# Kernel optimization log

Measured on AMD Instinct MI355X. Metric: run time of the kernel, lower is better.

The kernel has to match this reference:

```python
import jax, jax.numpy as jnp
import numpy as np

NUM_POINTS = 10


def _notaknot_spline_coeffs(points, values):
    """Replicates scipy.interpolate.CubicSpline (bc_type='not-a-knot').
    Solves for knot slopes s, then per-interval cubic coeffs in t = x - x_i:
      y = c3*t^3 + c2*t^2 + c1*t + c0.
    n = 10 so the dense n x n solve is negligible."""
    n = points.shape[0]
    dx = jnp.diff(points)                     # [n-1]
    slope = jnp.diff(values) / dx             # [n-1]

    A = jnp.zeros((n, n), dtype=points.dtype)
    b = jnp.zeros((n,), dtype=points.dtype)
    idx = jnp.arange(1, n - 1)
    # interior continuity-of-second-derivative rows
    A = A.at[idx, idx - 1].set(dx[1:])
    A = A.at[idx, idx].set(2.0 * (dx[:-1] + dx[1:]))
    A = A.at[idx, idx + 1].set(dx[:-1])
    b = b.at[idx].set(3.0 * (dx[1:] * slope[:-1] + dx[:-1] * slope[1:]))
    # not-a-knot boundary rows (as in scipy CubicSpline source)
    d0 = points[2] - points[0]
    A = A.at[0, 0].set(dx[1])
    A = A.at[0, 1].set(d0)
    b = b.at[0].set(((dx[0] + 2.0 * d0) * dx[1] * slope[0] + dx[0] ** 2 * slope[1]) / d0)
    dn = points[-1] - points[-3]
    A = A.at[-1, -1].set(dx[-2])
    A = A.at[-1, -2].set(dn)
    b = b.at[-1].set((dx[-1] ** 2 * slope[-2] + (2.0 * dn + dx[-1]) * dx[-2] * slope[-1]) / dn)

    s = jnp.linalg.solve(A, b)                # knot first derivatives
    t = (s[:-1] + s[1:] - 2.0 * slope) / dx
    c3 = t / dx
    c2 = (slope - s[:-1]) / dx - t
    c1 = s[:-1]
    c0 = values[:-1]
    return c3, c2, c1, c0


def setup_inputs() -> dict:
    key = jax.random.key(0)
    kx, kv = jax.random.split(key)
    x = jax.random.uniform(kx, (4096, 4096), dtype=jnp.float32)  # in [0,1) subset of [-1,1]
    points = jnp.linspace(-1.0, 1.0, NUM_POINTS, dtype=jnp.float32)  # nn.Parameter init
    values = jax.random.normal(kv, (NUM_POINTS,), dtype=jnp.float32)
    return {"x": x, "points": points, "values": values}


def reference(x, points, values):
    c3, c2, c1, c0 = _notaknot_spline_coeffs(points, values)
    xf = x.ravel()
    # interval search; clip -> end-interval polynomials extrapolate (scipy default)
    i = jnp.clip(jnp.searchsorted(points, xf, side='right') - 1, 0, points.shape[0] - 2)
    t = xf - points[i]
    y = ((c3[i] * t + c2[i]) * t + c1[i]) * t + c0[i]  # Horner
    return y.reshape(x.shape)
```

## Files before the change

kernel.cpp:

```cpp
#include <hip/hip_runtime.h>

typedef float float4v __attribute__((ext_vector_type(4)));

#define BLOCK 256

__device__ __forceinline__ void spline_setup(const float* __restrict__ points,
                                             const float* __restrict__ values,
                                             float2* s32, float2* s10, float* sm)
{
    float p[10], v[10];
#pragma unroll
    for (int k = 0; k < 10; ++k) { p[k] = points[k]; v[k] = values[k]; }
    float dx[9], sl[9];
#pragma unroll
    for (int k = 0; k < 9; ++k) { dx[k] = p[k + 1] - p[k]; sl[k] = (v[k + 1] - v[k]) / dx[k]; }

    float dg[10], lo[10], up[10], bb[10];
    float d0 = p[2] - p[0];
    dg[0] = dx[1]; up[0] = d0; lo[0] = 0.0f;
    bb[0] = ((dx[0] + 2.0f * d0) * dx[1] * sl[0] + dx[0] * dx[0] * sl[1]) / d0;
#pragma unroll
    for (int i = 1; i <= 8; ++i) {
        lo[i] = dx[i];
        dg[i] = 2.0f * (dx[i - 1] + dx[i]);
        up[i] = dx[i - 1];
        bb[i] = 3.0f * (dx[i] * sl[i - 1] + dx[i - 1] * sl[i]);
    }
    float dn = p[9] - p[7];
    lo[9] = dn; dg[9] = dx[7]; up[9] = 0.0f;
    bb[9] = (dx[8] * dx[8] * sl[7] + (2.0f * dn + dx[8]) * dx[7] * sl[8]) / dn;

    float cp[10], bp[10];
    cp[0] = up[0] / dg[0];
    bp[0] = bb[0] / dg[0];
#pragma unroll
    for (int i = 1; i <= 9; ++i) {
        float m = dg[i] - lo[i] * cp[i - 1];
        cp[i] = up[i] / m;
        bp[i] = (bb[i] - lo[i] * bp[i - 1]) / m;
    }
    float s[10];
    s[9] = bp[9];
#pragma unroll
    for (int i = 8; i >= 0; --i) s[i] = bp[i] - cp[i] * s[i + 1];

#pragma unroll
    for (int i = 0; i < 9; ++i) {
        float tt = (s[i] + s[i + 1] - 2.0f * sl[i]) / dx[i];
        float c3 = tt / dx[i];
        float c2 = (sl[i] - s[i]) / dx[i] - tt;
        float c1 = s[i];
        float c0 = v[i];
        float pi = p[i];
        float a3 = c3;
        float a2 = c2 - 3.0f * c3 * pi;
        float a1 = (3.0f * c3 * pi - 2.0f * c2) * pi + c1;
        float a0 = ((-c3 * pi + c2) * pi - c1) * pi + c0;
        s32[i] = make_float2(a3, a2);
        s10[i] = make_float2(a1, a0);
    }
    float scale = 9.0f / (p[9] - p[0]);
    sm[0] = scale;
    sm[1] = -p[0] * scale;
}

__device__ __forceinline__ int interval_idx(float xx, float scale, float off) {
    int i = (int)(xx * scale + off);
    i = i < 0 ? 0 : i;
    i = i > 8 ? 8 : i;
    return i;
}

__global__ __launch_bounds__(BLOCK) void spline_eval_kernel(
    const float* __restrict__ xin,
    const float* __restrict__ points,
    const float* __restrict__ values,
    float* __restrict__ out,
    int n4, int total)
{
    __shared__ float2 s32[9];
    __shared__ float2 s10[9];
    __shared__ float sm[2];

    if (threadIdx.x == 0) spline_setup(points, values, s32, s10, sm);
    __syncthreads();

    const float scale = sm[0], off = sm[1];

    const float4v* __restrict__ x4 = (const float4v*)xin;
    float4v* __restrict__ o4 = (float4v*)out;

    int idx = blockIdx.x * blockDim.x + threadIdx.x;
    int stride = gridDim.x * blockDim.x;

    for (int vi = idx; vi < n4; vi += stride) {
        float4v xv = __builtin_nontemporal_load(&x4[vi]);
        float4v yv;
#pragma unroll
        for (int j = 0; j < 4; ++j) {
            float xx = xv[j];
            int i = interval_idx(xx, scale, off);
            float2 h = s32[i];
            float2 l = s10[i];
            yv[j] = ((h.x * xx + h.y) * xx + l.x) * xx + l.y;
        }
        __builtin_nontemporal_store(yv, &o4[vi]);
    }

    int tail = n4 * 4;
    if (blockIdx.x == 0) {
        for (int e = tail + threadIdx.x; e < total; e += blockDim.x) {
            float xx = xin[e];
            int i = interval_idx(xx, scale, off);
            float2 h = s32[i];
            float2 l = s10[i];
            out[e] = ((h.x * xx + h.y) * xx + l.x) * xx + l.y;
        }
    }
}

extern "C" void kernel_launch(void* const* d_in, const int* in_sizes, int n_in,
                              void* d_out, int out_size, void* d_ws, size_t ws_size,
                              hipStream_t stream) {
    const float* x = (const float*)d_in[0];
    const float* points = (const float*)d_in[1];
    const float* values = (const float*)d_in[2];
    float* out = (float*)d_out;

    int total = out_size;
    int n4 = total / 4;

    const int block = BLOCK;
    const int grid = 2048;

    spline_eval_kernel<<<grid, block, 0, stream>>>(x, points, values, out, n4, total);
}
```

Measured before the change: 28.62 us.

## Add software-pipelined fixed-trip kernel with first load before spline setup

Adds a templated kernel with a compile-time trip count of 8 for the exact 4096x4096 size. It issues the first x load before thread 0 builds the coefficient table and prefetches the next float4 while evaluating the current one, hiding the setup and load latency. It also drops the nontemporal load and store hints in favour of plain accesses. The specialised path only runs when the element count matches grid*block*8; other sizes fall back to the generic loop.

```diff
diff --git a/kernel.cpp b/kernel.cpp
--- a/kernel.cpp
+++ b/kernel.cpp
@@ -64,14 +64,55 @@
     sm[1] = -p[0] * scale;
 }
 
-__device__ __forceinline__ int interval_idx(float xx, float scale, float off) {
+__device__ __forceinline__ float eval_one(float xx, float scale, float off,
+                                          const float2* s32, const float2* s10)
+{
     int i = (int)(xx * scale + off);
-    i = i < 0 ? 0 : i;
-    i = i > 8 ? 8 : i;
-    return i;
+    i = i < 0 ? 0 : (i > 8 ? 8 : i);
+    float2 h = s32[i];
+    float2 l = s10[i];
+    return ((h.x * xx + h.y) * xx + l.x) * xx + l.y;
 }
 
-__global__ __launch_bounds__(BLOCK) void spline_eval_kernel(
+template <int TRIPS>
+__global__ __launch_bounds__(BLOCK) void spline_eval_pipe(
+    const float* __restrict__ xin,
+    const float* __restrict__ points,
+    const float* __restrict__ values,
+    float* __restrict__ out)
+{
+    __shared__ float2 s32[9];
+    __shared__ float2 s10[9];
+    __shared__ float sm[2];
+
+    const float4v* __restrict__ x4 = (const float4v*)xin;
+    float4v* __restrict__ o4 = (float4v*)out;
+
+    const int stride = gridDim.x * BLOCK;
+    int vi = blockIdx.x * BLOCK + threadIdx.x;
+
+    float4v cur = x4[vi];
+
+    if (threadIdx.x == 0) spline_setup(points, values, s32, s10, sm);
+    __syncthreads();
+
+    const float scale = sm[0], off = sm[1];
+
+#pragma unroll
+    for (int k = 0; k < TRIPS; ++k) {
+        float4v nxt;
+        if (k + 1 < TRIPS) nxt = x4[vi + stride];
+        float4v yv;
+#pragma unroll
+        for (int j = 0; j < 4; ++j)
+            yv[j] = eval_one(cur[j], scale, off, s32, s10);
+        o4[vi] = yv;
+        vi += stride;
+        cur = nxt;
+    }
+}
+
+__global__ __launch_bounds__(BLOCK) void spline_eval_generic(
     const float* __restrict__ xin,
     const float* __restrict__ points,
     const float* __restrict__ values,
@@ -94,27 +135,18 @@
     int stride = gridDim.x * blockDim.x;
 
     for (int vi = idx; vi < n4; vi += stride) {
-        float4v xv = __builtin_nontemporal_load(&x4[vi]);
+        float4v xv = x4[vi];
         float4v yv;
 #pragma unroll
-        for (int j = 0; j < 4; ++j) {
-            float xx = xv[j];
-            int i = interval_idx(xx, scale, off);
-            float2 h = s32[i];
-            float2 l = s10[i];
-            yv[j] = ((h.x * xx + h.y) * xx + l.x) * xx + l.y;
-        }
-        __builtin_nontemporal_store(yv, &o4[vi]);
+        for (int j = 0; j < 4; ++j)
+            yv[j] = eval_one(xv[j], scale, off, s32, s10);
+        o4[vi] = yv;
     }
 
     int tail = n4 * 4;
     if (blockIdx.x == 0) {
         for (int e = tail + threadIdx.x; e < total; e += blockDim.x) {
-            float xx = xin[e];
-            int i = interval_idx(xx, scale, off);
-            float2 h = s32[i];
-            float2 l = s10[i];
-            out[e] = ((h.x * xx + h.y) * xx + l.x) * xx + l.y;
+            out[e] = eval_one(xin[e], scale, off, s32, s10);
         }
     }
 }
@@ -130,8 +162,12 @@
     int total = out_size;
     int n4 = total / 4;
 
-    const int block = BLOCK;
+    const int TRIPS = 8;
     const int grid = 2048;
 
-    spline_eval_kernel<<<grid, block, 0, stream>>>(x, points, values, out, n4, total);
+    if (total % 4 == 0 && n4 == grid * BLOCK * TRIPS) {
+        spline_eval_pipe<TRIPS><<<grid, BLOCK, 0, stream>>>(x, points, values, out);
+    } else {
+        spline_eval_generic<<<grid, BLOCK, 0, stream>>>(x, points, values, out, n4, total);
+    }
 }
```

After: 26.96 us, median of 2. -5.8%, faster.
